# Kernel tuning notes

Hardware: AMD Instinct MI355X
Metric: run time of the kernel (lower is better)

## Reference

```python
import jax, jax.numpy as jnp
import numpy as np
from math import pi

N_, C_, H_, W_, S_ = 32, 3, 224, 224, 16  # batch, channels, height, width, n_samples
INIT_VALUE = pi * 30 / 180.0  # dataset 'imagenet_r30' -> rotations in +-30 degrees


def setup_inputs() -> dict:
    key = jax.random.key(0)
    k1, k2 = jax.random.split(key)
    x = jax.random.normal(k1, (N_, C_, H_, W_), jnp.float32)
    # torch: cat((zeros(N), rand(N*S)*2-1)) * init_value, reshaped per-image: col 0 is identity
    u = jax.random.uniform(k2, (N_, S_), jnp.float32) * 2.0 - 1.0
    thetas = jnp.concatenate([jnp.zeros((N_, 1), jnp.float32), u * INIT_VALUE], axis=1)
    return {"x": x, "thetas": thetas}


def _rotation_grid(thetas, H, W, dtype):
    # F.affine_grid(align_corners=False): pixel-center normalized coords
    xs = ((jnp.arange(W, dtype=dtype) + 0.5) * 2.0 / W - 1.0)  # [W]
    ys = ((jnp.arange(H, dtype=dtype) + 0.5) * 2.0 / H - 1.0)  # [H]
    c = jnp.cos(thetas)[..., None, None]  # [N,S1,1,1]
    s = jnp.sin(thetas)[..., None, None]
    # theta matrix [[c,-s,0],[s,c,0]] applied to (x, y, 1)
    gx = c * xs[None, :] - s * ys[:, None]  # [N,S1,H,W]
    gy = s * xs[None, :] + c * ys[:, None]
    return gx, gy


def _grid_sample_bilinear_zeros(img, gx, gy):
    # img: [C,H,W]; gx,gy: [S1,H,W] normalized coords; align_corners=False, zero padding
    C, H, W = img.shape
    ix = ((gx + 1.0) * W - 1.0) * 0.5
    iy = ((gy + 1.0) * H - 1.0) * 0.5
    ix0f = jnp.floor(ix)
    iy0f = jnp.floor(iy)
    wx1 = ix - ix0f
    wy1 = iy - iy0f
    wx0 = 1.0 - wx1
    wy0 = 1.0 - wy1
    ix0 = ix0f.astype(jnp.int32)
    iy0 = iy0f.astype(jnp.int32)
    ix1 = ix0 + 1
    iy1 = iy0 + 1

    def gather(iy_, ix_, w):
        valid = (ix_ >= 0) & (ix_ < W) & (iy_ >= 0) & (iy_ < H)
        v = img[:, jnp.clip(iy_, 0, H - 1), jnp.clip(ix_, 0, W - 1)]  # [C,S1,H,W]
        return v * (w * valid.astype(img.dtype))[None]

    out = (gather(iy0, ix0, wy0 * wx0) + gather(iy0, ix1, wy0 * wx1)
           + gather(iy1, ix0, wy1 * wx0) + gather(iy1, ix1, wy1 * wx1))
    return jnp.transpose(out, (1, 0, 2, 3))  # [S1,C,H,W]


def reference(x, thetas):
    N, C, H, W = x.shape
    gx, gy = _rotation_grid(thetas, H, W, x.dtype)  # [N,S1,H,W] each
    out = jax.vmap(_grid_sample_bilinear_zeros)(x, gx, gy)  # [N,S1,C,H,W]
    return out
```

## Files before the change

### kernel.cpp

```cpp
#include <hip/hip_runtime.h>
#include <math.h>

namespace {
constexpr int N_  = 32;
constexpr int S1_ = 17;
constexpr int C_  = 3;
constexpr int H_  = 224;
constexpr int W_  = 224;
constexpr int HW_ = H_ * W_;
constexpr int TILE = 32;
constexpr int TPL  = W_ / TILE;
constexpr int LH   = 46;
constexpr int LWX  = 48;
constexpr int LSTR = 50;
constexpr int THREADS = 256;
}

__global__ __launch_bounds__(THREADS) void rot_bilinear_lds_kernel(
    const float* __restrict__ x,
    const float* __restrict__ thetas,
    float* __restrict__ out) {
  __shared__ float lds[LH * LSTR];

  const int ns = blockIdx.y;
  const int n  = ns / S1_;
  const int bx = blockIdx.x;
  const int c  = bx % C_;
  const int t  = bx / C_;
  const int h0 = (t / TPL) * TILE;
  const int w0 = (t % TPL) * TILE;

  const float theta = thetas[ns];
  float st, ct;
  sincosf(theta, &st, &ct);

  float fxmin = 1e30f, fymin = 1e30f;
#pragma unroll
  for (int cw = 0; cw < 2; ++cw) {
#pragma unroll
    for (int chh = 0; chh < 2; ++chh) {
      const float xs = ((w0 + cw * (TILE - 1)) + 0.5f) * (2.0f / W_) - 1.0f;
      const float ys = ((h0 + chh * (TILE - 1)) + 0.5f) * (2.0f / H_) - 1.0f;
      const float gx = ct * xs - st * ys;
      const float gy = st * xs + ct * ys;
      const float fx = ((gx + 1.0f) * W_ - 1.0f) * 0.5f;
      const float fy = ((gy + 1.0f) * H_ - 1.0f) * 0.5f;
      fxmin = fminf(fxmin, fx);
      fymin = fminf(fymin, fy);
    }
  }
  int rx0 = (int)floorf(fxmin - 0.1f);
  const int ry0 = (int)floorf(fymin - 0.1f);
  rx0 &= ~1;

  const float* __restrict__ img = x + (size_t)n * (C_ * HW_) + (size_t)c * HW_;
  const int tid = threadIdx.x;
  const bool interior =
      (rx0 >= 0) & (ry0 >= 0) & (rx0 + LWX <= W_) & (ry0 + LH <= H_);
  if (interior) {
    const float* __restrict__ p0 = img + ry0 * W_ + rx0;
    constexpr int NPAIR = LH * (LWX / 2);
    for (int i = tid; i < NPAIR; i += THREADS) {
      const int r  = i / (LWX / 2);
      const int c2 = i - r * (LWX / 2);
      const float2 v = *reinterpret_cast<const float2*>(p0 + r * W_ + 2 * c2);
      *reinterpret_cast<float2*>(&lds[r * LSTR + 2 * c2]) = v;
    }
  } else {
    for (int i = tid; i < LH * LWX; i += THREADS) {
      const int r = i / LWX;
      const int cc = i - r * LWX;
      const int gy = ry0 + r;
      const int gx = rx0 + cc;
      const bool in = (gx >= 0) & (gx < W_) & (gy >= 0) & (gy < H_);
      const int off = (in ? gy : 0) * W_ + (in ? gx : 0);
      const float m = in ? 1.0f : 0.0f;
      lds[r * LSTR + cc] = img[off] * m;
    }
  }
  __syncthreads();

  const int row = tid >> 3;
  const int col = (tid & 7) * 4;
  const int h = h0 + row;
  const int w_base = w0 + col;
  const float ys = (h + 0.5f) * (2.0f / H_) - 1.0f;
  const float xs0 = (w_base + 0.5f) * (2.0f / W_) - 1.0f;
  const float gx0 = ct * xs0 - st * ys;
  const float gy0 = st * xs0 + ct * ys;
  float fx = ((gx0 + 1.0f) * W_ - 1.0f) * 0.5f;
  float fy = ((gy0 + 1.0f) * H_ - 1.0f) * 0.5f;

  float r0[4];
#pragma unroll
  for (int k = 0; k < 4; ++k) {
    const float fx0 = floorf(fx);
    const float fy0 = floorf(fy);
    const float wx1 = fx - fx0;
    const float wy1 = fy - fy0;
    const float wx0 = 1.0f - wx1;
    const float wy0 = 1.0f - wy1;
    const int lx = (int)fx0 - rx0;
    const int ly = (int)fy0 - ry0;
    const int base = ly * LSTR + lx;
    const float w00 = wy0 * wx0, w01 = wy0 * wx1;
    const float w10 = wy1 * wx0, w11 = wy1 * wx1;
    r0[k] = w00 * lds[base]        + w01 * lds[base + 1] +
            w10 * lds[base + LSTR] + w11 * lds[base + LSTR + 1];
    fx += ct;
    fy += st;
  }

  float* __restrict__ o = out + (size_t)ns * (C_ * HW_) + (size_t)c * HW_ +
                          (size_t)h * W_ + w_base;
  *reinterpret_cast<float4*>(o) = make_float4(r0[0], r0[1], r0[2], r0[3]);
}

extern "C" void kernel_launch(void* const* d_in, const int* in_sizes, int n_in,
                              void* d_out, int out_size, void* d_ws,
                              size_t ws_size, hipStream_t stream) {
  const float* x      = (const float*)d_in[0];
  const float* thetas = (const float*)d_in[1];
  float* out          = (float*)d_out;

  dim3 grid(TPL * TPL * C_, N_ * S1_);
  rot_bilinear_lds_kernel<<<grid, THREADS, 0, stream>>>(x, thetas, out);
}
```

Baseline: 435.7 us.

## Use persistent blocks with register-prefetched LDS tiles pipelining gather and compute

Replaces the one-block-per-tile grid with a fixed set of 2048 persistent blocks. Each block walks a contiguous range of tiles and channels, prefetching the next source window into registers while the current window is sampled from LDS. The aim is to overlap global loads with bilinear compute and reuse the tile geometry and sincos across the three channels. It also changes the LDS stride to 49, switches from float2 to scalar loads, and drops rx0 alignment. The cost is extra barriers per item, more register pressure from the prefetch slots, and less block-level parallelism.

```diff
diff --git a/kernel.cpp b/kernel.cpp
--- a/kernel.cpp
+++ b/kernel.cpp
@@ -10,37 +10,46 @@
 constexpr int HW_ = H_ * W_;
 constexpr int TILE = 32;
 constexpr int TPL  = W_ / TILE;
+constexpr int TILES_PER_PLANE = TPL * TPL;
+constexpr int NTILES = N_ * S1_ * TILES_PER_PLANE;
 constexpr int LH   = 46;
 constexpr int LWX  = 48;
-constexpr int LSTR = 50;
+constexpr int LSTR = 49;
+constexpr int NELEM = LH * LWX;
 constexpr int THREADS = 256;
+constexpr int SLOTS = (NELEM + THREADS - 1) / THREADS;
+constexpr int NBLK  = 2048;
 }
 
-__global__ __launch_bounds__(THREADS) void rot_bilinear_lds_kernel(
-    const float* __restrict__ x,
-    const float* __restrict__ thetas,
-    float* __restrict__ out) {
-  __shared__ float lds[LH * LSTR];
+struct TileCtx {
+  const float* img;
+  int ns;
+  int h0, w0;
+  int rx0, ry0;
+  int interior;
+  float ct, st;
+};
 
-  const int ns = blockIdx.y;
-  const int n  = ns / S1_;
-  const int bx = blockIdx.x;
-  const int c  = bx % C_;
-  const int t  = bx / C_;
-  const int h0 = (t / TPL) * TILE;
-  const int w0 = (t % TPL) * TILE;
-
-  const float theta = thetas[ns];
+static __device__ inline TileCtx tile_coords(int tile,
+                                             const float* __restrict__ x,
+                                             const float* __restrict__ thetas) {
+  TileCtx tc;
+  const int ns = tile / TILES_PER_PLANE;
+  const int t  = tile - ns * TILES_PER_PLANE;
+  tc.ns = ns;
+  const int n = ns / S1_;
+  tc.h0 = (t / TPL) * TILE;
+  tc.w0 = (t % TPL) * TILE;
   float st, ct;
-  sincosf(theta, &st, &ct);
-
+  sincosf(thetas[ns], &st, &ct);
+  tc.ct = ct; tc.st = st;
   float fxmin = 1e30f, fymin = 1e30f;
 #pragma unroll
   for (int cw = 0; cw < 2; ++cw) {
 #pragma unroll
     for (int chh = 0; chh < 2; ++chh) {
-      const float xs = ((w0 + cw * (TILE - 1)) + 0.5f) * (2.0f / W_) - 1.0f;
-      const float ys = ((h0 + chh * (TILE - 1)) + 0.5f) * (2.0f / H_) - 1.0f;
+      const float xs = ((tc.w0 + cw * (TILE - 1)) + 0.5f) * (2.0f / W_) - 1.0f;
+      const float ys = ((tc.h0 + chh * (TILE - 1)) + 0.5f) * (2.0f / H_) - 1.0f;
       const float gx = ct * xs - st * ys;
       const float gy = st * xs + ct * ys;
       const float fx = ((gx + 1.0f) * W_ - 1.0f) * 0.5f;
@@ -49,71 +58,122 @@
       fymin = fminf(fymin, fy);
     }
   }
-  int rx0 = (int)floorf(fxmin - 0.1f);
-  const int ry0 = (int)floorf(fymin - 0.1f);
-  rx0 &= ~1;
+  tc.rx0 = (int)floorf(fxmin - 0.1f);
+  tc.ry0 = (int)floorf(fymin - 0.1f);
+  tc.interior = (tc.rx0 >= 0) & (tc.ry0 >= 0) &
+                (tc.rx0 + LWX <= W_) & (tc.ry0 + LH <= H_);
+  tc.img = x + (size_t)n * (C_ * HW_);
+  return tc;
+}
 
-  const float* __restrict__ img = x + (size_t)n * (C_ * HW_) + (size_t)c * HW_;
-  const int tid = threadIdx.x;
-  const bool interior =
-      (rx0 >= 0) & (ry0 >= 0) & (rx0 + LWX <= W_) & (ry0 + LH <= H_);
-  if (interior) {
-    const float* __restrict__ p0 = img + ry0 * W_ + rx0;
-    constexpr int NPAIR = LH * (LWX / 2);
-    for (int i = tid; i < NPAIR; i += THREADS) {
-      const int r  = i / (LWX / 2);
-      const int c2 = i - r * (LWX / 2);
-      const float2 v = *reinterpret_cast<const float2*>(p0 + r * W_ + 2 * c2);
-      *reinterpret_cast<float2*>(&lds[r * LSTR + 2 * c2]) = v;
+static __device__ inline void prefetch_item(const TileCtx& tc, int ch, int tid,
+                                            float va[SLOTS]) {
+  const float* __restrict__ p = tc.img + (size_t)ch * HW_;
+  if (tc.interior) {
+#pragma unroll
+    for (int s = 0; s < SLOTS; ++s) {
+      const int idx = tid + s * THREADS;
+      float v = 0.0f;
+      if (idx < NELEM) {
+        const int r = idx / LWX;
+        const int c = idx - r * LWX;
+        v = p[(tc.ry0 + r) * W_ + (tc.rx0 + c)];
+      }
+      va[s] = v;
     }
   } else {
-    for (int i = tid; i < LH * LWX; i += THREADS) {
-      const int r = i / LWX;
-      const int cc = i - r * LWX;
-      const int gy = ry0 + r;
-      const int gx = rx0 + cc;
-      const bool in = (gx >= 0) & (gx < W_) & (gy >= 0) & (gy < H_);
-      const int off = (in ? gy : 0) * W_ + (in ? gx : 0);
-      const float m = in ? 1.0f : 0.0f;
-      lds[r * LSTR + cc] = img[off] * m;
+#pragma unroll
+    for (int s = 0; s < SLOTS; ++s) {
+      const int idx = tid + s * THREADS;
+      float v = 0.0f;
+      if (idx < NELEM) {
+        const int r = idx / LWX;
+        const int c = idx - r * LWX;
+        const int gy = tc.ry0 + r;
+        const int gx = tc.rx0 + c;
+        const bool in = (gx >= 0) & (gx < W_) & (gy >= 0) & (gy < H_);
+        const int off = (in ? gy : 0) * W_ + (in ? gx : 0);
+        v = p[off] * (in ? 1.0f : 0.0f);
+      }
+      va[s] = v;
     }
   }
-  __syncthreads();
+}
 
-  const int row = tid >> 3;
-  const int col = (tid & 7) * 4;
-  const int h = h0 + row;
-  const int w_base = w0 + col;
-  const float ys = (h + 0.5f) * (2.0f / H_) - 1.0f;
-  const float xs0 = (w_base + 0.5f) * (2.0f / W_) - 1.0f;
-  const float gx0 = ct * xs0 - st * ys;
-  const float gy0 = st * xs0 + ct * ys;
-  float fx = ((gx0 + 1.0f) * W_ - 1.0f) * 0.5f;
-  float fy = ((gy0 + 1.0f) * H_ - 1.0f) * 0.5f;
+__global__ __launch_bounds__(THREADS) void rot_bilinear_pipe_kernel(
+    const float* __restrict__ x,
+    const float* __restrict__ thetas,
+    float* __restrict__ out) {
+  __shared__ float lds[LH * LSTR];
 
-  float r0[4];
+  const int tid = threadIdx.x;
+  const int b   = blockIdx.x;
+  const int t0  = (int)((long)b * NTILES / NBLK);
+  const int t1  = (int)((long)(b + 1) * NTILES / NBLK);
+  const int nitems = (t1 - t0) * C_;
+
+  const int row    = tid >> 3;
+  const int col    = (tid & 7) * 4;
+
+  float va[SLOTS];
+  TileCtx tc_pre = tile_coords(t0, x, thetas);
+  prefetch_item(tc_pre, 0, tid, va);
+  TileCtx tc;
+
+  for (int i = 0; i < nitems; ++i) {
+    __syncthreads();
 #pragma unroll
-  for (int k = 0; k < 4; ++k) {
-    const float fx0 = floorf(fx);
-    const float fy0 = floorf(fy);
-    const float wx1 = fx - fx0;
-    const float wy1 = fy - fy0;
-    const float wx0 = 1.0f - wx1;
-    const float wy0 = 1.0f - wy1;
-    const int lx = (int)fx0 - rx0;
-    const int ly = (int)fy0 - ry0;
-    const int base = ly * LSTR + lx;
-    const float w00 = wy0 * wx0, w01 = wy0 * wx1;
-    const float w10 = wy1 * wx0, w11 = wy1 * wx1;
-    r0[k] = w00 * lds[base]        + w01 * lds[base + 1] +
-            w10 * lds[base + LSTR] + w11 * lds[base + LSTR + 1];
-    fx += ct;
-    fy += st;
+    for (int s = 0; s < SLOTS; ++s) {
+      const int idx = tid + s * THREADS;
+      if (idx < NELEM) {
+        const int r = idx / LWX;
+        const int c = idx - r * LWX;
+        lds[r * LSTR + c] = va[s];
+      }
+    }
+    tc = tc_pre;
+    const int ch = i - (i / C_) * C_;
+    __syncthreads();
+
+    if (i + 1 < nitems) {
+      const int ch_n = (i + 1) - ((i + 1) / C_) * C_;
+      if (ch_n == 0) tc_pre = tile_coords(t0 + (i + 1) / C_, x, thetas);
+      prefetch_item(tc_pre, ch_n, tid, va);
+    }
+
+    const int h = tc.h0 + row;
+    const int w_base = tc.w0 + col;
+    const float ys = (h + 0.5f) * (2.0f / H_) - 1.0f;
+    const float xs0 = (w_base + 0.5f) * (2.0f / W_) - 1.0f;
+    const float gx0 = tc.ct * xs0 - tc.st * ys;
+    const float gy0 = tc.st * xs0 + tc.ct * ys;
+    float fx = ((gx0 + 1.0f) * W_ - 1.0f) * 0.5f;
+    float fy = ((gy0 + 1.0f) * H_ - 1.0f) * 0.5f;
+
+    float r0[4];
+#pragma unroll
+    for (int k = 0; k < 4; ++k) {
+      const float fx0 = floorf(fx);
+      const float fy0 = floorf(fy);
+      const float wx1 = fx - fx0;
+      const float wy1 = fy - fy0;
+      const float wx0 = 1.0f - wx1;
+      const float wy0 = 1.0f - wy1;
+      const int lx = (int)fx0 - tc.rx0;
+      const int ly = (int)fy0 - tc.ry0;
+      const int base = ly * LSTR + lx;
+      const float w00 = wy0 * wx0, w01 = wy0 * wx1;
+      const float w10 = wy1 * wx0, w11 = wy1 * wx1;
+      r0[k] = w00 * lds[base]        + w01 * lds[base + 1] +
+              w10 * lds[base + LSTR] + w11 * lds[base + LSTR + 1];
+      fx += tc.ct;
+      fy += tc.st;
+    }
+
+    float* __restrict__ o = out + (size_t)tc.ns * (C_ * HW_) +
+                            (size_t)ch * HW_ + (size_t)h * W_ + w_base;
+    *reinterpret_cast<float4*>(o) = make_float4(r0[0], r0[1], r0[2], r0[3]);
   }
-
-  float* __restrict__ o = out + (size_t)ns * (C_ * HW_) + (size_t)c * HW_ +
-                          (size_t)h * W_ + w_base;
-  *reinterpret_cast<float4*>(o) = make_float4(r0[0], r0[1], r0[2], r0[3]);
 }
 
 extern "C" void kernel_launch(void* const* d_in, const int* in_sizes, int n_in,
@@ -123,6 +183,6 @@
   const float* thetas = (const float*)d_in[1];
   float* out          = (float*)d_out;
 
-  dim3 grid(TPL * TPL * C_, N_ * S1_);
-  rot_bilinear_lds_kernel<<<grid, THREADS, 0, stream>>>(x, thetas, out);
+  rot_bilinear_pipe_kernel<<<dim3(NBLK), dim3(THREADS), 0, stream>>>(
+      x, thetas, out);
 }
```

Measured after the change: 471.0 us. +8.1%, slower.
